# Performance work log

Hardware: AMD Instinct MI355X
Metric: run time of the kernel (lower is better)

The kernel has to match this reference:

```python
import jax, jax.numpy as jnp
import numpy as np

N, E = 50000, 600000
IN_DIM, H, D = 256, 4, 128
NEG_SLOPE = 0.2


def setup_inputs() -> dict:
    key = jax.random.key(0)
    ks = jax.random.split(key, 9)
    x = jax.random.normal(ks[0], (N, IN_DIM), dtype=jnp.float32)
    src = jax.random.randint(ks[1], (E,), 0, N, dtype=jnp.int32)
    dst = jax.random.randint(ks[2], (E,), 0, N, dtype=jnp.int32)
    # layer 0: in=256 -> H*D=512; layer 1: in=H*D=512 -> H*D=512
    s0 = 1.0 / np.sqrt(IN_DIM)
    s1 = 1.0 / np.sqrt(H * D)
    W0 = jax.random.normal(ks[3], (IN_DIM, H * D), dtype=jnp.float32) * s0
    al0 = jax.random.normal(ks[4], (H, D), dtype=jnp.float32) * s1
    ar0 = jax.random.normal(ks[5], (H, D), dtype=jnp.float32) * s1
    W1 = jax.random.normal(ks[6], (H * D, H * D), dtype=jnp.float32) * s1
    al1 = jax.random.normal(ks[7], (H, D), dtype=jnp.float32) * s1
    ar1 = jax.random.normal(ks[8], (H, D), dtype=jnp.float32) * s1
    return {"x": x, "src": src, "dst": dst,
            "W0": W0, "al0": al0, "ar0": ar0,
            "W1": W1, "al1": al1, "ar1": ar1}


def gat_conv(x, W, al, ar, src, dst):
    """One DGL-style GATConv layer. x:[N,in] -> out:[N,H,D] (post relu)."""
    h = (x @ W).reshape(N, H, D)                       # fc, no bias
    el = jnp.sum(h * al, axis=-1)                      # [N,H]
    er = jnp.sum(h * ar, axis=-1)                      # [N,H]
    e = jax.nn.leaky_relu(el[src] + er[dst], NEG_SLOPE)  # [E,H]
    # edge softmax over incoming edges of each dst node (numerically stable)
    m = jax.ops.segment_max(e, dst, num_segments=N)    # [N,H]
    m = jnp.where(jnp.isfinite(m), m, 0.0)             # empty segments -> -inf
    ex = jnp.exp(e - m[dst])                           # [E,H]
    denom = jax.ops.segment_sum(ex, dst, num_segments=N)  # [N,H]
    alpha = ex / denom[dst]                            # [E,H]
    msg = alpha[:, :, None] * h[src]                   # [E,H,D]
    rst = jax.ops.segment_sum(msg, dst, num_segments=N)  # [N,H,D]
    return jax.nn.relu(rst)                            # activation=F.relu


def reference(x, src, dst, W0, al0, ar0, W1, al1, ar1):
    h = gat_conv(x, W0, al0, ar0, src, dst)            # [N,H,D]
    h = h.reshape(N, H * D)                            # flatten(1)
    h = gat_conv(h, W1, al1, ar1, src, dst)            # [N,H,D]
    return h.mean(axis=1)                              # mean over heads -> [N,D]
```

## Files before the change

### kernel.cpp

```cpp
#include <hip/hip_runtime.h>

#define NN 50000
#define NE 600000
#define DD 128
#define HD 512
#define NB 196

typedef unsigned short u16;
typedef __attribute__((ext_vector_type(8))) short short8;
typedef __attribute__((ext_vector_type(4))) float floatx4;

__device__ inline float b2f(u16 u) {
  return __uint_as_float(((unsigned int)u) << 16);
}
__device__ inline u16 f2b(float f) {
  unsigned int u = __float_as_uint(f);
  u = u + 0x7FFFu + ((u >> 16) & 1u);
  return (u16)(u >> 16);
}

__device__ inline void load_lds16(const u16* g, u16* l) {
  __builtin_amdgcn_global_load_lds(
      (const __attribute__((address_space(1))) unsigned int*)(uintptr_t)g,
      (__attribute__((address_space(3))) unsigned int*)(uintptr_t)l,
      16, 0, 0);
}

__global__ void zero_k(int* __restrict__ p, int n) {
  int i = blockIdx.x * 256 + threadIdx.x;
  if (i < n) p[i] = 0;
}

__global__ void transpose_k(const float* __restrict__ W, u16* __restrict__ Wt, int K) {
  int idx = blockIdx.x * 256 + threadIdx.x;
  if (idx >= K * 512) return;
  int k = idx >> 9, n = idx & 511;
  Wt[n * K + k] = f2b(W[idx]);
}

__global__ void count_k(const int* __restrict__ dst, int* __restrict__ counts) {
  int e = blockIdx.x * 256 + threadIdx.x;
  if (e < NE) atomicAdd(&counts[dst[e]], 1);
}

__global__ __launch_bounds__(256) void blockscan_k(const int* __restrict__ counts,
                                                   int* __restrict__ rowp,
                                                   int* __restrict__ bsums) {
  __shared__ int tmp[256];
  int t = threadIdx.x;
  int i = blockIdx.x * 256 + t;
  int v = (i < NN) ? counts[i] : 0;
  tmp[t] = v;
  __syncthreads();
  for (int off = 1; off < 256; off <<= 1) {
    int u = (t >= off) ? tmp[t - off] : 0;
    __syncthreads();
    tmp[t] += u;
    __syncthreads();
  }
  if (i < NN) rowp[i] = tmp[t] - v;
  if (t == 255) bsums[blockIdx.x] = tmp[t];
}

__global__ __launch_bounds__(256) void bscan_k(const int* __restrict__ bsums,
                                               int* __restrict__ boffs) {
  __shared__ int tmp[256];
  int t = threadIdx.x;
  int v = (t < NB) ? bsums[t] : 0;
  tmp[t] = v;
  __syncthreads();
  for (int off = 1; off < 256; off <<= 1) {
    int u = (t >= off) ? tmp[t - off] : 0;
    __syncthreads();
    tmp[t] += u;
    __syncthreads();
  }
  if (t < NB) boffs[t] = tmp[t] - v;
}

__global__ void addoff_k(int* __restrict__ rowp, int* __restrict__ cursor,
                         const int* __restrict__ boffs) {
  int i = blockIdx.x * 256 + threadIdx.x;
  if (i < NN) {
    int v = rowp[i] + boffs[blockIdx.x];
    rowp[i] = v;
    cursor[i] = v;
  }
  if (i == 0) rowp[NN] = NE;
}

__global__ void scatter_k(const int* __restrict__ src, const int* __restrict__ dst,
                          int* __restrict__ cursor, int* __restrict__ csrs) {
  int e = blockIdx.x * 256 + threadIdx.x;
  if (e < NE) {
    int d = dst[e];
    int pos = atomicAdd(&cursor[d], 1);
    csrs[pos] = src[e];
  }
}

template <int K, bool A_F32>
__global__ __launch_bounds__(512) void gemm_el_er(
    const void* __restrict__ Ap, const u16* __restrict__ Wt,
    const float* __restrict__ al, const float* __restrict__ ar,
    u16* __restrict__ h, float* __restrict__ el, float* __restrict__ er) {
  __shared__ u16 Wt_s[512 * 32];

  const int tid = threadIdx.x;
  const int w = tid >> 6, lane = tid & 63, quad = lane >> 4, l16 = lane & 15;
  const int rg = w >> 1, cg = w & 1;
  const int bm = blockIdx.x;

  floatx4 acc[16] = {};

  const int rowA = bm * 64 + rg * 16 + l16;
  const long arow = (rowA < NN) ? rowA : (NN - 1);

  const int drow = lane >> 2;
  const int q8 = ((lane & 3) ^ ((lane >> 3) & 3)) * 8;
  const int p4 = (quad ^ ((l16 >> 1) & 3)) * 8;

  for (int k0 = 0; k0 < K; k0 += 32) {
#pragma unroll
    for (int rr = 0; rr < 4; ++rr) {
      const int rbase = rr * 128 + w * 16;
      load_lds16(Wt + (long)(rbase + drow) * K + k0 + q8, Wt_s + rbase * 32);
    }
    short8 af;
    if (A_F32) {
      const float* Af = (const float*)Ap;
      floatx4 v0 = *(const floatx4*)(Af + arow * K + k0 + quad * 8);
      floatx4 v1 = *(const floatx4*)(Af + arow * K + k0 + quad * 8 + 4);
      u16 tmp[8];
#pragma unroll
      for (int j = 0; j < 4; ++j) tmp[j] = f2b(v0[j]);
#pragma unroll
      for (int j = 0; j < 4; ++j) tmp[4 + j] = f2b(v1[j]);
      af = *(short8*)tmp;
    } else {
      af = *(const short8*)((const u16*)Ap + arow * K + k0 + quad * 8);
    }
    __syncthreads();
#pragma unroll
    for (int ct = 0; ct < 16; ++ct) {
      short8 bf = *(const short8*)(Wt_s + (cg * 256 + ct * 16 + l16) * 32 + p4);
      acc[ct] = __builtin_amdgcn_mfma_f32_16x16x32_bf16(af, bf, acc[ct], 0, 0, 0);
    }
    __syncthreads();
  }

  float alv[16], arv[16];
#pragma unroll
  for (int ct = 0; ct < 16; ++ct) {
    int col = cg * 256 + ct * 16 + l16;
    alv[ct] = al[col];
    arv[ct] = ar[col];
  }
#pragma unroll
  for (int reg = 0; reg < 4; ++reg) {
    const int r = bm * 64 + rg * 16 + quad * 4 + reg;
    float pel[2] = {0.f, 0.f}, per_[2] = {0.f, 0.f};
#pragma unroll
    for (int ct = 0; ct < 16; ++ct) {
      int hh = ct >> 3;
      float v = acc[ct][reg];
      pel[hh] += v * alv[ct];
      per_[hh] += v * arv[ct];
    }
#pragma unroll
    for (int m = 1; m < 16; m <<= 1) {
      pel[0] += __shfl_xor(pel[0], m, 64);
      pel[1] += __shfl_xor(pel[1], m, 64);
      per_[0] += __shfl_xor(per_[0], m, 64);
      per_[1] += __shfl_xor(per_[1], m, 64);
    }
    if (r < NN) {
#pragma unroll
      for (int ct = 0; ct < 16; ++ct)
        h[(long)r * HD + cg * 256 + ct * 16 + l16] = f2b(acc[ct][reg]);
      if (l16 == 0) {
        el[r * 4 + cg * 2] = pel[0];
        el[r * 4 + cg * 2 + 1] = pel[1];
        er[r * 4 + cg * 2] = per_[0];
        er[r * 4 + cg * 2 + 1] = per_[1];
      }
    }
  }
}

template <int MODE>
__global__ __launch_bounds__(256) void aggregate(
    const u16* __restrict__ h, const float* __restrict__ el,
    const float* __restrict__ er, const int* __restrict__ rowp,
    const int* __restrict__ csrs, u16* __restrict__ ob, float* __restrict__ of) {
  __shared__ float w_s[4][64][4];
  const int wv = threadIdx.x >> 6, lane = threadIdx.x & 63;
  const int n = blockIdx.x * 4 + wv;
  if (n >= NN) return;
  const int base = rowp[n];
  const int deg = rowp[n + 1] - base;
  const int head = lane >> 4;

  if (deg == 0) {
    if (MODE == 0) {
      short8 z = {};
      __builtin_nontemporal_store(z, (short8*)(ob + (long)n * HD + lane * 8));
    } else if (lane < 16) {
      floatx4 z = {};
      __builtin_nontemporal_store(z, (floatx4*)(of + (long)n * DD + lane * 8));
      __builtin_nontemporal_store(z, (floatx4*)(of + (long)n * DD + lane * 8 + 4));
    }
    return;
  }

  const floatx4 er4 = *(const floatx4*)(er + n * 4);

  float acc[8] = {0.f, 0.f, 0.f, 0.f, 0.f, 0.f, 0.f, 0.f};
  float sm0 = 0.f, sm1 = 0.f, sm2 = 0.f, sm3 = 0.f;

  for (int c0 = 0; c0 < deg; c0 += 64) {
    const int cnt = min(deg - c0, 64);

    const int l = c0 + lane;
    const int idx = csrs[base + ((l < deg) ? l : (deg - 1))];
    const floatx4 el4 = *(const floatx4*)(el + (long)idx * 4);
    floatx4 w4;
#pragma unroll
    for (int j = 0; j < 4; ++j) {
      float e = el4[j] + er4[j];
      e = (e > 0.f) ? e : 0.2f * e;
      w4[j] = (l < deg) ? __expf(e) : 0.f;
    }
    sm0 += w4[0];
    sm1 += w4[1];
    sm2 += w4[2];
    sm3 += w4[3];
    *(floatx4*)(&w_s[wv][lane][0]) = w4;

    for (int i = 0; i < cnt; i += 8) {
      short8 hv[8];
#pragma unroll
      for (int u = 0; u < 8; ++u) {
        const int s = __builtin_amdgcn_readlane(idx, i + u);
        hv[u] = *(const short8*)(h + (long)s * HD + lane * 8);
      }
#pragma unroll
      for (int u = 0; u < 8; ++u) {
        const float w = w_s[wv][i + u][head];
#pragma unroll
        for (int j = 0; j < 8; ++j) acc[j] += w * b2f((u16)hv[u][j]);
      }
    }
  }

#pragma unroll
  for (int m = 1; m < 64; m <<= 1) {
    sm0 += __shfl_xor(sm0, m, 64);
    sm1 += __shfl_xor(sm1, m, 64);
    sm2 += __shfl_xor(sm2, m, 64);
    sm3 += __shfl_xor(sm3, m, 64);
  }
  const float sm = (head == 0) ? sm0 : (head == 1) ? sm1 : (head == 2) ? sm2 : sm3;

  const float inv = 1.f / sm;
#pragma unroll
  for (int j = 0; j < 8; ++j) acc[j] = fmaxf(acc[j] * inv, 0.f);

  if (MODE == 0) {
    u16 ub[8];
#pragma unroll
    for (int j = 0; j < 8; ++j) ub[j] = f2b(acc[j]);
    __builtin_nontemporal_store(*(short8*)ub, (short8*)(ob + (long)n * HD + lane * 8));
  } else {
#pragma unroll
    for (int j = 0; j < 8; ++j) acc[j] += __shfl_xor(acc[j], 16, 64);
#pragma unroll
    for (int j = 0; j < 8; ++j) acc[j] += __shfl_xor(acc[j], 32, 64);
    if (lane < 16) {
      floatx4 o0, o1;
#pragma unroll
      for (int j = 0; j < 4; ++j) o0[j] = acc[j] * 0.25f;
#pragma unroll
      for (int j = 0; j < 4; ++j) o1[j] = acc[4 + j] * 0.25f;
      __builtin_nontemporal_store(o0, (floatx4*)(of + (long)n * DD + lane * 8));
      __builtin_nontemporal_store(o1, (floatx4*)(of + (long)n * DD + lane * 8 + 4));
    }
  }
}

extern "C" void kernel_launch(void* const* d_in, const int* in_sizes, int n_in,
                              void* d_out, int out_size, void* d_ws, size_t ws_size,
                              hipStream_t stream) {
  const float* x = (const float*)d_in[0];
  const int* src = (const int*)d_in[1];
  const int* dst = (const int*)d_in[2];
  const float* W0 = (const float*)d_in[3];
  const float* al0 = (const float*)d_in[4];
  const float* ar0 = (const float*)d_in[5];
  const float* W1 = (const float*)d_in[6];
  const float* al1 = (const float*)d_in[7];
  const float* ar1 = (const float*)d_in[8];
  float* out = (float*)d_out;

  char* p = (char*)d_ws;
  u16* h = (u16*)p;        p += (size_t)NN * HD * 2;
  u16* rst0 = (u16*)p;     p += (size_t)NN * HD * 2;
  float* el = (float*)p;   p += (size_t)NN * 4 * 4;
  float* er = (float*)p;   p += (size_t)NN * 4 * 4;
  u16* Wt0 = (u16*)p;      p += 512 * 256 * 2;
  u16* Wt1 = (u16*)p;      p += 512 * 512 * 2;
  int* counts = (int*)p;   p += (size_t)NN * 4;
  int* cursor = (int*)p;   p += (size_t)NN * 4;
  int* rowp = (int*)p;     p += (size_t)(NN + 1) * 4;
  int* bsums = (int*)p;    p += 256 * 4;
  int* boffs = (int*)p;    p += 256 * 4;
  int* csrs = (int*)p;     p += (size_t)NE * 4;

  zero_k<<<NB, 256, 0, stream>>>(counts, NN);
  count_k<<<(NE + 255) / 256, 256, 0, stream>>>(dst, counts);
  blockscan_k<<<NB, 256, 0, stream>>>(counts, rowp, bsums);
  bscan_k<<<1, 256, 0, stream>>>(bsums, boffs);
  addoff_k<<<NB, 256, 0, stream>>>(rowp, cursor, boffs);
  scatter_k<<<(NE + 255) / 256, 256, 0, stream>>>(src, dst, cursor, csrs);
  transpose_k<<<(256 * 512 + 255) / 256, 256, 0, stream>>>(W0, Wt0, 256);
  transpose_k<<<(512 * 512 + 255) / 256, 256, 0, stream>>>(W1, Wt1, 512);

  const int gblocks = (NN + 63) / 64;
  gemm_el_er<256, true><<<gblocks, 512, 0, stream>>>(x, Wt0, al0, ar0, h, el, er);
  aggregate<0><<<(NN + 3) / 4, 256, 0, stream>>>(h, el, er, rowp, csrs, rst0, nullptr);
  gemm_el_er<512, false><<<gblocks, 512, 0, stream>>>(rst0, Wt1, al1, ar1, h, el, er);
  aggregate<1><<<(NN + 3) / 4, 256, 0, stream>>>(h, el, er, rowp, csrs, nullptr, out);
}
```

Baseline: 475.2 us.

## Split aggregation into 16 feature-column chunks per node with atomic head-mean output

```diff
diff --git a/kernel.cpp b/kernel.cpp
--- a/kernel.cpp
+++ b/kernel.cpp
@@ -189,101 +189,82 @@
 }
 
 template <int MODE>
-__global__ __launch_bounds__(256) void aggregate(
+__global__ __launch_bounds__(256) void aggregate_chunk(
     const u16* __restrict__ h, const float* __restrict__ el,
     const float* __restrict__ er, const int* __restrict__ rowp,
     const int* __restrict__ csrs, u16* __restrict__ ob, float* __restrict__ of) {
-  __shared__ float w_s[4][64][4];
+  __shared__ float w_s[4][64];
+  __shared__ int is_s[4][64];
+  const int b = blockIdx.x;
+  const int half = b / 25000;
+  const int chunk = (b & 7) + half * 8;
+  const int nodeblk = (b % 25000) >> 3;
   const int wv = threadIdx.x >> 6, lane = threadIdx.x & 63;
-  const int n = blockIdx.x * 4 + wv;
-  if (n >= NN) return;
-  const int base = rowp[n];
-  const int deg = rowp[n + 1] - base;
-  const int head = lane >> 4;
-
-  if (deg == 0) {
+  const int hc = chunk >> 2;
+  const int eg = lane >> 4, cl = lane & 15;
+  const long coff = chunk * 32 + cl * 2;
+
+  for (int k = 0; k < 4; ++k) {
+    const int n = nodeblk * 16 + wv * 4 + k;
+    const int base = rowp[n];
+    const int deg = rowp[n + 1] - base;
+    if (deg == 0) {
+      if (MODE == 0 && lane < 16)
+        __builtin_nontemporal_store(0u, (unsigned*)(ob + (long)n * HD + coff));
+      continue;
+    }
+    const float er_h = er[n * 4 + hc];
+    float acc0 = 0.f, acc1 = 0.f, sm = 0.f;
+    for (int c0 = 0; c0 < deg; c0 += 64) {
+      const int l = c0 + lane;
+      const int idx =
+          __builtin_nontemporal_load(csrs + base + ((l < deg) ? l : (deg - 1)));
+      float e = el[idx * 4 + hc] + er_h;
+      e = (e > 0.f) ? e : 0.2f * e;
+      const float w = (l < deg) ? __expf(e) : 0.f;
+      sm += w;
+      w_s[wv][lane] = w;
+      is_s[wv][lane] = idx;
+      const int cnt = (deg - c0 < 64) ? (deg - c0) : 64;
+      for (int i = 0; i < cnt; i += 16) {
+        int s4[4];
+        float wt[4];
+        unsigned v4[4];
+#pragma unroll
+        for (int u = 0; u < 4; ++u) {
+          s4[u] = is_s[wv][i + u * 4 + eg];
+          wt[u] = w_s[wv][i + u * 4 + eg];
+        }
+#pragma unroll
+        for (int u = 0; u < 4; ++u)
+          v4[u] = *(const unsigned*)(h + (long)s4[u] * HD + coff);
+#pragma unroll
+        for (int u = 0; u < 4; ++u) {
+          acc0 += wt[u] * __uint_as_float(v4[u] << 16);
+          acc1 += wt[u] * __uint_as_float(v4[u] & 0xFFFF0000u);
+        }
+      }
+    }
+    acc0 += __shfl_xor(acc0, 16, 64);
+    acc0 += __shfl_xor(acc0, 32, 64);
+    acc1 += __shfl_xor(acc1, 16, 64);
+    acc1 += __shfl_xor(acc1, 32, 64);
+#pragma unroll
+    for (int m = 1; m < 64; m <<= 1) sm += __shfl_xor(sm, m, 64);
+    const float inv = 1.f / sm;
+    const float v0 = fmaxf(acc0 * inv, 0.f);
+    const float v1 = fmaxf(acc1 * inv, 0.f);
     if (MODE == 0) {
-      short8 z = {};
-      __builtin_nontemporal_store(z, (short8*)(ob + (long)n * HD + lane * 8));
-    } else if (lane < 16) {
-      floatx4 z = {};
-      __builtin_nontemporal_store(z, (floatx4*)(of + (long)n * DD + lane * 8));
-      __builtin_nontemporal_store(z, (floatx4*)(of + (long)n * DD + lane * 8 + 4));
-    }
-    return;
-  }
-
-  const floatx4 er4 = *(const floatx4*)(er + n * 4);
-
-  float acc[8] = {0.f, 0.f, 0.f, 0.f, 0.f, 0.f, 0.f, 0.f};
-  float sm0 = 0.f, sm1 = 0.f, sm2 = 0.f, sm3 = 0.f;
-
-  for (int c0 = 0; c0 < deg; c0 += 64) {
-    const int cnt = min(deg - c0, 64);
-
-    const int l = c0 + lane;
-    const int idx = csrs[base + ((l < deg) ? l : (deg - 1))];
-    const floatx4 el4 = *(const floatx4*)(el + (long)idx * 4);
-    floatx4 w4;
-#pragma unroll
-    for (int j = 0; j < 4; ++j) {
-      float e = el4[j] + er4[j];
-      e = (e > 0.f) ? e : 0.2f * e;
-      w4[j] = (l < deg) ? __expf(e) : 0.f;
-    }
-    sm0 += w4[0];
-    sm1 += w4[1];
-    sm2 += w4[2];
-    sm3 += w4[3];
-    *(floatx4*)(&w_s[wv][lane][0]) = w4;
-
-    for (int i = 0; i < cnt; i += 8) {
-      short8 hv[8];
-#pragma unroll
-      for (int u = 0; u < 8; ++u) {
-        const int s = __builtin_amdgcn_readlane(idx, i + u);
-        hv[u] = *(const short8*)(h + (long)s * HD + lane * 8);
+      if (lane < 16) {
+        unsigned u = (unsigned)f2b(v0) | ((unsigned)f2b(v1) << 16);
+        __builtin_nontemporal_store(u, (unsigned*)(ob + (long)n * HD + coff));
       }
-#pragma unroll
-      for (int u = 0; u < 8; ++u) {
-        const float w = w_s[wv][i + u][head];
-#pragma unroll
-        for (int j = 0; j < 8; ++j) acc[j] += w * b2f((u16)hv[u][j]);
+    } else {
+      if (lane < 16) {
+        float* o = of + (long)n * DD + (chunk & 3) * 32 + cl * 2;
+        atomicAdd(o, v0 * 0.25f);
+        atomicAdd(o + 1, v1 * 0.25f);
       }
-    }
-  }
-
-#pragma unroll
-  for (int m = 1; m < 64; m <<= 1) {
-    sm0 += __shfl_xor(sm0, m, 64);
-    sm1 += __shfl_xor(sm1, m, 64);
-    sm2 += __shfl_xor(sm2, m, 64);
-    sm3 += __shfl_xor(sm3, m, 64);
-  }
-  const float sm = (head == 0) ? sm0 : (head == 1) ? sm1 : (head == 2) ? sm2 : sm3;
-
-  const float inv = 1.f / sm;
-#pragma unroll
-  for (int j = 0; j < 8; ++j) acc[j] = fmaxf(acc[j] * inv, 0.f);
-
-  if (MODE == 0) {
-    u16 ub[8];
-#pragma unroll
-    for (int j = 0; j < 8; ++j) ub[j] = f2b(acc[j]);
-    __builtin_nontemporal_store(*(short8*)ub, (short8*)(ob + (long)n * HD + lane * 8));
-  } else {
-#pragma unroll
-    for (int j = 0; j < 8; ++j) acc[j] += __shfl_xor(acc[j], 16, 64);
-#pragma unroll
-    for (int j = 0; j < 8; ++j) acc[j] += __shfl_xor(acc[j], 32, 64);
-    if (lane < 16) {
-      floatx4 o0, o1;
-#pragma unroll
-      for (int j = 0; j < 4; ++j) o0[j] = acc[j] * 0.25f;
-#pragma unroll
-      for (int j = 0; j < 4; ++j) o1[j] = acc[4 + j] * 0.25f;
-      __builtin_nontemporal_store(o0, (floatx4*)(of + (long)n * DD + lane * 8));
-      __builtin_nontemporal_store(o1, (floatx4*)(of + (long)n * DD + lane * 8 + 4));
     }
   }
 }
@@ -326,8 +307,10 @@
   transpose_k<<<(512 * 512 + 255) / 256, 256, 0, stream>>>(W1, Wt1, 512);
 
   const int gblocks = (NN + 63) / 64;
+  const int ablocks = 50000;
   gemm_el_er<256, true><<<gblocks, 512, 0, stream>>>(x, Wt0, al0, ar0, h, el, er);
-  aggregate<0><<<(NN + 3) / 4, 256, 0, stream>>>(h, el, er, rowp, csrs, rst0, nullptr);
+  aggregate_chunk<0><<<ablocks, 256, 0, stream>>>(h, el, er, rowp, csrs, rst0, nullptr);
   gemm_el_er<512, false><<<gblocks, 512, 0, stream>>>(rst0, Wt1, al1, ar1, h, el, er);
-  aggregate<1><<<(NN + 3) / 4, 256, 0, stream>>>(h, el, er, rowp, csrs, nullptr, out);
-}
+  zero_k<<<(NN * DD + 255) / 256, 256, 0, stream>>>((int*)out, NN * DD);
+  aggregate_chunk<1><<<ablocks, 256, 0, stream>>>(h, el, er, rowp, csrs, nullptr, out);
+}
```

Measured after the change: 836.5 us. +76.0%, slower.

## Double-buffer weight tiles in GEMM with manual vmcnt waits

Applied to the files above, without the earlier changes.

```diff
diff --git a/kernel.cpp b/kernel.cpp
--- a/kernel.cpp
+++ b/kernel.cpp
@@ -104,7 +104,7 @@
     const void* __restrict__ Ap, const u16* __restrict__ Wt,
     const float* __restrict__ al, const float* __restrict__ ar,
     u16* __restrict__ h, float* __restrict__ el, float* __restrict__ er) {
-  __shared__ u16 Wt_s[512 * 32];
+  __shared__ u16 Wt_s[2][512 * 32];
 
   const int tid = threadIdx.x;
   const int w = tid >> 6, lane = tid & 63, quad = lane >> 4, l16 = lane & 15;
@@ -120,34 +120,95 @@
   const int q8 = ((lane & 3) ^ ((lane >> 3) & 3)) * 8;
   const int p4 = (quad ^ ((l16 >> 1) & 3)) * 8;
 
-  for (int k0 = 0; k0 < K; k0 += 32) {
-#pragma unroll
-    for (int rr = 0; rr < 4; ++rr) {
-      const int rbase = rr * 128 + w * 16;
-      load_lds16(Wt + (long)(rbase + drow) * K + k0 + q8, Wt_s + rbase * 32);
-    }
-    short8 af;
-    if (A_F32) {
-      const float* Af = (const float*)Ap;
-      floatx4 v0 = *(const floatx4*)(Af + arow * K + k0 + quad * 8);
-      floatx4 v1 = *(const floatx4*)(Af + arow * K + k0 + quad * 8 + 4);
-      u16 tmp[8];
-#pragma unroll
-      for (int j = 0; j < 4; ++j) tmp[j] = f2b(v0[j]);
-#pragma unroll
-      for (int j = 0; j < 4; ++j) tmp[4 + j] = f2b(v1[j]);
-      af = *(short8*)tmp;
-    } else {
-      af = *(const short8*)((const u16*)Ap + arow * K + k0 + quad * 8);
-    }
-    __syncthreads();
-#pragma unroll
-    for (int ct = 0; ct < 16; ++ct) {
-      short8 bf = *(const short8*)(Wt_s + (cg * 256 + ct * 16 + l16) * 32 + p4);
-      acc[ct] = __builtin_amdgcn_mfma_f32_16x16x32_bf16(af, bf, acc[ct], 0, 0, 0);
-    }
-    __syncthreads();
-  }
+  const float* Af = (const float*)Ap;
+  const u16* Ab = (const u16*)Ap;
+
+#define ISSUE_DMA(kk, sel)                                                  \
+  {                                                                         \
+    _Pragma("unroll") for (int rr = 0; rr < 4; ++rr) {                      \
+      const int rbase = rr * 128 + w * 16;                                  \
+      load_lds16(Wt + (long)(rbase + drow) * K + (kk) + q8,                 \
+                 &Wt_s[sel][rbase * 32]);                                   \
+    }                                                                       \
+  }
+
+  floatx4 a0A, a1A, a0B, a1B;
+  short8 rawA, rawB;
+
+#define ISSUE_A(kk, a0r, a1r, rawr)                                         \
+  {                                                                         \
+    if (A_F32) {                                                            \
+      a0r = *(const floatx4*)(Af + arow * K + (kk) + quad * 8);             \
+      a1r = *(const floatx4*)(Af + arow * K + (kk) + quad * 8 + 4);         \
+    } else {                                                                \
+      rawr = *(const short8*)(Ab + arow * K + (kk) + quad * 8);             \
+    }                                                                       \
+  }
+
+#define CVT_A(af, a0r, a1r, rawr)                                           \
+  short8 af;                                                                \
+  {                                                                         \
+    if (A_F32) {                                                            \
+      u16 tmp[8];                                                           \
+      _Pragma("unroll") for (int j = 0; j < 4; ++j) tmp[j] = f2b(a0r[j]);   \
+      _Pragma("unroll") for (int j = 0; j < 4; ++j) tmp[4 + j] = f2b(a1r[j]); \
+      af = *(short8*)tmp;                                                   \
+    } else {                                                                \
+      af = rawr;                                                            \
+    }                                                                       \
+  }
+
+#define WAIT_PREV()                                                         \
+  {                                                                         \
+    if (A_F32)                                                              \
+      asm volatile("s_waitcnt vmcnt(6)" ::: "memory");                      \
+    else                                                                    \
+      asm volatile("s_waitcnt vmcnt(5)" ::: "memory");                      \
+  }
+
+  const int T = K / 32;
+
+  ISSUE_A(0, a0A, a1A, rawA);
+  ISSUE_DMA(0, 0);
+
+  for (int t = 0; t < T; t += 2) {
+    {
+      const int k1 = (t + 1) * 32;
+      ISSUE_A(k1, a0B, a1B, rawB);
+      ISSUE_DMA(k1, 1);
+      WAIT_PREV();
+      __builtin_amdgcn_s_barrier();
+      CVT_A(af, a0A, a1A, rawA);
+#pragma unroll
+      for (int ct = 0; ct < 16; ++ct) {
+        short8 bf = *(const short8*)(&Wt_s[0][(cg * 256 + ct * 16 + l16) * 32 + p4]);
+        acc[ct] = __builtin_amdgcn_mfma_f32_16x16x32_bf16(af, bf, acc[ct], 0, 0, 0);
+      }
+      __builtin_amdgcn_sched_barrier(0);
+      __builtin_amdgcn_s_barrier();
+    }
+    {
+      const int t2 = (t + 2 < T) ? t + 2 : T - 1;
+      const int k2 = t2 * 32;
+      ISSUE_A(k2, a0A, a1A, rawA);
+      ISSUE_DMA(k2, 0);
+      WAIT_PREV();
+      __builtin_amdgcn_s_barrier();
+      CVT_A(af, a0B, a1B, rawB);
+#pragma unroll
+      for (int ct = 0; ct < 16; ++ct) {
+        short8 bf = *(const short8*)(&Wt_s[1][(cg * 256 + ct * 16 + l16) * 32 + p4]);
+        acc[ct] = __builtin_amdgcn_mfma_f32_16x16x32_bf16(af, bf, acc[ct], 0, 0, 0);
+      }
+      __builtin_amdgcn_sched_barrier(0);
+      __builtin_amdgcn_s_barrier();
+    }
+  }
+
+#undef ISSUE_DMA
+#undef ISSUE_A
+#undef CVT_A
+#undef WAIT_PREV
 
   float alv[16], arv[16];
 #pragma unroll
@@ -204,7 +265,7 @@
   if (deg == 0) {
     if (MODE == 0) {
       short8 z = {};
-      __builtin_nontemporal_store(z, (short8*)(ob + (long)n * HD + lane * 8));
+      *(short8*)(ob + (long)n * HD + lane * 8) = z;
     } else if (lane < 16) {
       floatx4 z = {};
       __builtin_nontemporal_store(z, (floatx4*)(of + (long)n * DD + lane * 8));
@@ -270,7 +331,7 @@
     u16 ub[8];
 #pragma unroll
     for (int j = 0; j < 8; ++j) ub[j] = f2b(acc[j]);
-    __builtin_nontemporal_store(*(short8*)ub, (short8*)(ob + (long)n * HD + lane * 8));
+    *(short8*)(ob + (long)n * HD + lane * 8) = *(short8*)ub;
   } else {
 #pragma unroll
     for (int j = 0; j < 8; ++j) acc[j] += __shfl_xor(acc[j], 16, 64);
```

New measurement: 466.3 us. No clear change (-1.9%).
